# Optimization experiments

Hardware: AMD Instinct MI355X
Metric: run time of the kernel (lower is better)

## Reference

```python
import jax, jax.numpy as jnp
import numpy as np

B, N, DIM, T, H, DH = 4, 2048, 512, 16, 8, 64
EPS = 1e-5


def setup_inputs() -> dict:
    key = jax.random.key(0)
    ks = jax.random.split(key, 7)
    x = jax.random.normal(ks[0], (B, N, DIM), dtype=jnp.float32)
    # time-distance matrix, e.g. months between scans, in [0, 24)
    R = jax.random.uniform(ks[1], (B, T, T), dtype=jnp.float32) * 24.0
    gamma = jnp.ones((DIM,), dtype=jnp.float32)
    beta = jnp.zeros((DIM,), dtype=jnp.float32)
    W_qkv = jax.random.normal(ks[2], (DIM, 3 * H * DH), dtype=jnp.float32) * 0.02
    W_out = jax.random.normal(ks[3], (H * DH, DIM), dtype=jnp.float32) * 0.02
    a = jax.random.uniform(ks[4], (H,), dtype=jnp.float32)          # torch.rand(heads)
    c = 12.0 * jax.random.uniform(ks[5], (H,), dtype=jnp.float32)   # 12 * torch.rand(heads)
    return {"x": x, "R": R, "gamma": gamma, "beta": beta,
            "W_qkv": W_qkv, "W_out": W_out, "a": a, "c": c}


def reference(x, R, gamma, beta, W_qkv, W_out, a, c):
    b, n, dim = x.shape
    t = R.shape[-1]
    num_patches = n // t
    scale = DH ** -0.5

    # LayerNorm
    mu = jnp.mean(x, axis=-1, keepdims=True)
    var = jnp.mean(jnp.square(x - mu), axis=-1, keepdims=True)
    xn = (x - mu) * jax.lax.rsqrt(var + EPS) * gamma + beta

    # QKV projection -> [b, h, n, d]
    qkv = xn @ W_qkv  # [b, n, 3*h*d]
    q, k, v = jnp.split(qkv, 3, axis=-1)
    def to_heads(z):
        return z.reshape(b, n, H, DH).transpose(0, 2, 1, 3)
    q, k, v = to_heads(q), to_heads(k), to_heads(v)

    # attention scores with ReLU then learned sigmoid time-decay mask
    dots = jnp.einsum('bhnd,bhmd->bhnm', q, k) * scale
    dots = jax.nn.relu(dots)

    # flipped-sigmoid decay: 1 / (1 + exp(|a|*R - |c|)), per head  -> [b, h, t, t]
    decay = 1.0 / (1.0 + jnp.exp(jnp.abs(a)[None, :, None, None] * R[:, None, :, :]
                                 - jnp.abs(c)[None, :, None, None]))
    # expand timepoint mask to token resolution (repeat_interleave on both axes)
    decay = jnp.repeat(jnp.repeat(decay, num_patches, axis=2), num_patches, axis=3)

    attn = jax.nn.softmax(dots * decay, axis=-1)
    out = jnp.einsum('bhnm,bhmd->bhnd', attn, v)
    out = out.transpose(0, 2, 1, 3).reshape(b, n, H * DH)
    return out @ W_out  # dropout is identity at eval
```

## Files before the change

kernel.cpp:

```cpp
#include <hip/hip_runtime.h>
#include <math.h>

#define B_   4
#define N_   2048
#define DIM_ 512
#define T_   16
#define H_   8
#define DH_  64

typedef unsigned short ushort_t;
typedef __attribute__((ext_vector_type(8))) short bf16x8;
typedef __attribute__((ext_vector_type(16))) float f32x16;

__device__ inline ushort_t bf16_rn(float x) {
  unsigned u = __builtin_bit_cast(unsigned, x);
  u += 0x7FFFu + ((u >> 16) & 1u);
  return (ushort_t)(u >> 16);
}
__device__ inline float bf16f(ushort_t h) {
  return __builtin_bit_cast(float, (unsigned)h << 16);
}
__device__ inline unsigned pack2(ushort_t a, ushort_t b) {
  return (unsigned)a | ((unsigned)b << 16);
}
__device__ inline void split2(float x, ushort_t &h, ushort_t &l) {
  h = bf16_rn(x);
  l = bf16_rn(x - bf16f(h));
}

__global__ __launch_bounds__(256) void transpose_split_kernel(
    const float* __restrict__ src, ushort_t* __restrict__ dh,
    ushort_t* __restrict__ dl, int K, int Nn) {
  __shared__ float Ts[64][68];
  int tid = threadIdx.x;
  int n0 = blockIdx.x * 64;
  int k0 = blockIdx.y * 64;
#pragma unroll
  for (int it = 0; it < 4; ++it) {
    int idx = tid + it * 256;
    int r = idx >> 4, c4 = (idx & 15) * 4;
    *(float4*)&Ts[r][c4] = *(const float4*)&src[(size_t)(k0 + r) * Nn + n0 + c4];
  }
  __syncthreads();
#pragma unroll
  for (int it = 0; it < 2; ++it) {
    int idx = tid + it * 256;
    int n = idx >> 3, kc = (idx & 7) * 8;
    ushort_t hs[8], ls[8];
#pragma unroll
    for (int j = 0; j < 8; ++j) split2(Ts[kc + j][n], hs[j], ls[j]);
    uint4 uh, ul;
    uh.x = pack2(hs[0], hs[1]); uh.y = pack2(hs[2], hs[3]);
    uh.z = pack2(hs[4], hs[5]); uh.w = pack2(hs[6], hs[7]);
    ul.x = pack2(ls[0], ls[1]); ul.y = pack2(ls[2], ls[3]);
    ul.z = pack2(ls[4], ls[5]); ul.w = pack2(ls[6], ls[7]);
    size_t o = (size_t)(n0 + n) * K + k0 + kc;
    *(uint4*)&dh[o] = uh;
    *(uint4*)&dl[o] = ul;
  }
}

__global__ __launch_bounds__(256) void ln_xn_kernel(
    const float* __restrict__ x, const float* __restrict__ gamma,
    const float* __restrict__ beta, ushort_t* __restrict__ xnh,
    ushort_t* __restrict__ xnl) {
  int row  = blockIdx.x * 4 + (threadIdx.x >> 6);
  int lane = threadIdx.x & 63;
  const float4* xr = (const float4*)(x + (size_t)row * DIM_);
  float4 v0 = xr[lane * 2 + 0];
  float4 v1 = xr[lane * 2 + 1];
  float s  = v0.x + v0.y + v0.z + v0.w + v1.x + v1.y + v1.z + v1.w;
  float ss = v0.x*v0.x + v0.y*v0.y + v0.z*v0.z + v0.w*v0.w
           + v1.x*v1.x + v1.y*v1.y + v1.z*v1.z + v1.w*v1.w;
#pragma unroll
  for (int off = 32; off > 0; off >>= 1) {
    s  += __shfl_xor(s, off);
    ss += __shfl_xor(ss, off);
  }
  float mu  = s * (1.0f / DIM_);
  float var = ss * (1.0f / DIM_) - mu * mu;
  float rstd = rsqrtf(var + 1e-5f);
  float4 g0 = *(const float4*)&gamma[lane * 8];
  float4 g1 = *(const float4*)&gamma[lane * 8 + 4];
  float4 b0 = *(const float4*)&beta[lane * 8];
  float4 b1 = *(const float4*)&beta[lane * 8 + 4];
  float xv[8] = {v0.x, v0.y, v0.z, v0.w, v1.x, v1.y, v1.z, v1.w};
  float gv[8] = {g0.x, g0.y, g0.z, g0.w, g1.x, g1.y, g1.z, g1.w};
  float bv[8] = {b0.x, b0.y, b0.z, b0.w, b1.x, b1.y, b1.z, b1.w};
  ushort_t hs[8], ls[8];
#pragma unroll
  for (int j = 0; j < 8; ++j) {
    float xn = (xv[j] - mu) * rstd * gv[j] + bv[j];
    split2(xn, hs[j], ls[j]);
  }
  uint4 uh, ul;
  uh.x = pack2(hs[0], hs[1]); uh.y = pack2(hs[2], hs[3]);
  uh.z = pack2(hs[4], hs[5]); uh.w = pack2(hs[6], hs[7]);
  ul.x = pack2(ls[0], ls[1]); ul.y = pack2(ls[2], ls[3]);
  ul.z = pack2(ls[4], ls[5]); ul.w = pack2(ls[6], ls[7]);
  size_t o = (size_t)row * DIM_ + lane * 8;
  *(uint4*)&xnh[o] = uh;
  *(uint4*)&xnl[o] = ul;
}

__global__ __launch_bounds__(256) void qkv_gemm_mfma(
    const ushort_t* __restrict__ xnh, const ushort_t* __restrict__ xnl,
    const ushort_t* __restrict__ wth, const ushort_t* __restrict__ wtl,
    ushort_t* __restrict__ qh, ushort_t* __restrict__ ql,
    ushort_t* __restrict__ kho, ushort_t* __restrict__ klo,
    ushort_t* __restrict__ vt) {
  __shared__ ushort_t Ah[128 * 40], Al[128 * 40], Bh[128 * 40], Bl[128 * 40];
  int tid = threadIdx.x;
  int w = tid >> 6, lane = tid & 63, l31 = lane & 31, g = lane >> 5;
  int wm = w >> 1, wn = w & 1;
  int n0 = blockIdx.x * 128;
  int m0 = blockIdx.y * 128;

  f32x16 acc[2][2];
#pragma unroll
  for (int i = 0; i < 2; ++i)
#pragma unroll
    for (int j = 0; j < 2; ++j)
#pragma unroll
      for (int e = 0; e < 16; ++e) acc[i][j][e] = 0.0f;

  int fm[2], fc[2];
#pragma unroll
  for (int it = 0; it < 2; ++it) {
    int f = tid + it * 256;
    fm[it] = f >> 2;
    fc[it] = (f & 3) * 8;
  }

#pragma unroll 1
  for (int kt = 0; kt < 16; ++kt) {
    __syncthreads();
#pragma unroll
    for (int it = 0; it < 2; ++it) {
      size_t ao = (size_t)(m0 + fm[it]) * 512 + kt * 32 + fc[it];
      size_t bo = (size_t)(n0 + fm[it]) * 512 + kt * 32 + fc[it];
      uint4 tah = *(const uint4*)&xnh[ao];
      uint4 tal = *(const uint4*)&xnl[ao];
      uint4 tbh = *(const uint4*)&wth[bo];
      uint4 tbl = *(const uint4*)&wtl[bo];
      int o = fm[it] * 40 + fc[it];
      *(uint4*)&Ah[o] = tah;
      *(uint4*)&Al[o] = tal;
      *(uint4*)&Bh[o] = tbh;
      *(uint4*)&Bl[o] = tbl;
    }
    __syncthreads();
#pragma unroll
    for (int kc = 0; kc < 2; ++kc) {
      int off = kc * 16 + 8 * g;
      bf16x8 afh[2], afl[2], bfh[2], bfl[2];
#pragma unroll
      for (int rb = 0; rb < 2; ++rb) {
        int r = (wm * 64 + rb * 32 + l31) * 40 + off;
        afh[rb] = *(const bf16x8*)&Ah[r];
        afl[rb] = *(const bf16x8*)&Al[r];
      }
#pragma unroll
      for (int cb = 0; cb < 2; ++cb) {
        int r = (wn * 64 + cb * 32 + l31) * 40 + off;
        bfh[cb] = *(const bf16x8*)&Bh[r];
        bfl[cb] = *(const bf16x8*)&Bl[r];
      }
#pragma unroll
      for (int rb = 0; rb < 2; ++rb)
#pragma unroll
        for (int cb = 0; cb < 2; ++cb) {
          acc[rb][cb] = __builtin_amdgcn_mfma_f32_32x32x16_bf16(afh[rb], bfh[cb], acc[rb][cb], 0, 0, 0);
          acc[rb][cb] = __builtin_amdgcn_mfma_f32_32x32x16_bf16(afh[rb], bfl[cb], acc[rb][cb], 0, 0, 0);
          acc[rb][cb] = __builtin_amdgcn_mfma_f32_32x32x16_bf16(afl[rb], bfh[cb], acc[rb][cb], 0, 0, 0);
        }
    }
  }

  int part = n0 >> 9;
#pragma unroll
  for (int rb = 0; rb < 2; ++rb) {
    int m_base = m0 + wm * 64 + rb * 32;
#pragma unroll
    for (int cb = 0; cb < 2; ++cb) {
      int n_g = n0 + wn * 64 + cb * 32 + l31;
      int rem = n_g & 511, hh = rem >> 6, d = rem & 63;
      if (part == 2) {
#pragma unroll
        for (int grp = 0; grp < 4; ++grp) {
          int m_g = m_base + grp * 8 + 4 * g;
          int bb = m_g >> 11, tok = m_g & 2047;
          uint2 pk;
          pk.x = pack2(bf16_rn(acc[rb][cb][grp * 4 + 0]), bf16_rn(acc[rb][cb][grp * 4 + 1]));
          pk.y = pack2(bf16_rn(acc[rb][cb][grp * 4 + 2]), bf16_rn(acc[rb][cb][grp * 4 + 3]));
          *(uint2*)&vt[((size_t)(bb * 8 + hh) * 64 + d) * 2048 + tok] = pk;
        }
      } else {
        float sc = (part == 0) ? 0.125f : 1.0f;
        ushort_t* dsth = (part == 0) ? qh : kho;
        ushort_t* dstl = (part == 0) ? ql : klo;
#pragma unroll
        for (int reg = 0; reg < 16; ++reg) {
          int row = (reg & 3) + 8 * (reg >> 2) + 4 * g;
          int m_g = m_base + row;
          int bb = m_g >> 11, tok = m_g & 2047;
          ushort_t hi, lo;
          split2(acc[rb][cb][reg] * sc, hi, lo);
          size_t addr = ((size_t)(bb * 8 + hh) * 2048 + tok) * 64 + d;
          dsth[addr] = hi;
          dstl[addr] = lo;
        }
      }
    }
  }
}

__global__ __launch_bounds__(256) void attn_mfma(
    const ushort_t* __restrict__ qh, const ushort_t* __restrict__ ql,
    const ushort_t* __restrict__ kho, const ushort_t* __restrict__ klo,
    const ushort_t* __restrict__ vt, const float* __restrict__ R,
    const float* __restrict__ a, const float* __restrict__ c,
    ushort_t* __restrict__ aoh, ushort_t* __restrict__ aol) {
  __shared__ ushort_t KhS[64 * 72], KlS[64 * 72], VtS[64 * 72], PS[64 * 72];
  __shared__ float rsLDS[2][64];

  int tid = threadIdx.x;
  int w = tid >> 6, lane = tid & 63, l31 = lane & 31, g = lane >> 5;
  int qhalf = w >> 1, khalf = w & 1;
  int bh = blockIdx.x;
  int qt = blockIdx.y;
  int b = bh >> 3, h = bh & 7;
  float aab = fabsf(a[h]);
  float cab = fabsf(c[h]);

  size_t qoff = ((size_t)bh * 2048 + qt * 64 + qhalf * 32 + l31) * 64;
  bf16x8 qfh[4], qfl[4];
#pragma unroll
  for (int d0i = 0; d0i < 4; ++d0i) {
    qfh[d0i] = *(const bf16x8*)&qh[qoff + d0i * 16 + 8 * g];
    qfl[d0i] = *(const bf16x8*)&ql[qoff + d0i * 16 + 8 * g];
  }

  int frow[2], fcc[2];
#pragma unroll
  for (int it = 0; it < 2; ++it) {
    int f = tid + it * 256;
    frow[it] = f >> 3;
    fcc[it] = (f & 7) * 8;
  }
  const ushort_t* kbase = kho + (size_t)bh * 2048 * 64;
  const ushort_t* lbase = klo + (size_t)bh * 2048 * 64;
  const ushort_t* vbase = vt + (size_t)bh * 64 * 2048;

  f32x16 oacc;
#pragma unroll
  for (int i = 0; i < 16; ++i) oacc[i] = 0.0f;
  float rs_acc[16] = {};
  int ti = qt >> 1;

#pragma unroll 1
  for (int kt = 0; kt < 32; ++kt) {
    __syncthreads();
#pragma unroll
    for (int it = 0; it < 2; ++it) {
      uint4 tk = *(const uint4*)&kbase[(size_t)(kt * 64 + frow[it]) * 64 + fcc[it]];
      uint4 tl = *(const uint4*)&lbase[(size_t)(kt * 64 + frow[it]) * 64 + fcc[it]];
      uint4 tv = *(const uint4*)&vbase[(size_t)frow[it] * 2048 + kt * 64 + fcc[it]];
      int o = frow[it] * 72 + fcc[it];
      *(uint4*)&KhS[o] = tk;
      *(uint4*)&KlS[o] = tl;
      *(uint4*)&VtS[o] = tv;
    }
    __syncthreads();

    f32x16 sacc;
#pragma unroll
    for (int i = 0; i < 16; ++i) sacc[i] = 0.0f;
    int krow = (khalf * 32 + l31) * 72;
#pragma unroll
    for (int d0i = 0; d0i < 4; ++d0i) {
      int off = krow + d0i * 16 + 8 * g;
      bf16x8 kfh = *(const bf16x8*)&KhS[off];
      bf16x8 kfl = *(const bf16x8*)&KlS[off];
      sacc = __builtin_amdgcn_mfma_f32_32x32x16_bf16(qfh[d0i], kfh, sacc, 0, 0, 0);
      sacc = __builtin_amdgcn_mfma_f32_32x32x16_bf16(qfh[d0i], kfl, sacc, 0, 0, 0);
      sacc = __builtin_amdgcn_mfma_f32_32x32x16_bf16(qfl[d0i], kfh, sacc, 0, 0, 0);
    }

    float Rv = R[b * (T_ * T_) + ti * T_ + (kt >> 1)];
    float dec = 1.0f / (1.0f + __expf(aab * Rv - cab));
#pragma unroll
    for (int reg = 0; reg < 16; ++reg) {
      float pv = __expf(fmaxf(sacc[reg], 0.0f) * dec);
      rs_acc[reg] += pv;
      int row = (reg & 3) + 8 * (reg >> 2) + 4 * g;
      PS[(qhalf * 32 + row) * 72 + khalf * 32 + l31] = bf16_rn(pv);
    }
    __syncthreads();

#pragma unroll
    for (int k0i = 0; k0i < 4; ++k0i) {
      bf16x8 pf = *(const bf16x8*)&PS[(qhalf * 32 + l31) * 72 + k0i * 16 + 8 * g];
      bf16x8 vf = *(const bf16x8*)&VtS[(khalf * 32 + l31) * 72 + k0i * 16 + 8 * g];
      oacc = __builtin_amdgcn_mfma_f32_32x32x16_bf16(pf, vf, oacc, 0, 0, 0);
    }
  }

#pragma unroll
  for (int reg = 0; reg < 16; ++reg) {
    float vsum = rs_acc[reg];
    vsum += __shfl_xor(vsum, 1);
    vsum += __shfl_xor(vsum, 2);
    vsum += __shfl_xor(vsum, 4);
    vsum += __shfl_xor(vsum, 8);
    vsum += __shfl_xor(vsum, 16);
    rs_acc[reg] = vsum;
  }
  if (l31 == 0) {
#pragma unroll
    for (int reg = 0; reg < 16; ++reg) {
      int row = (reg & 3) + 8 * (reg >> 2) + 4 * g;
      rsLDS[khalf][qhalf * 32 + row] = rs_acc[reg];
    }
  }
  __syncthreads();

#pragma unroll
  for (int reg = 0; reg < 16; ++reg) {
    int row = (reg & 3) + 8 * (reg >> 2) + 4 * g;
    int qg = qhalf * 32 + row;
    float invs = 1.0f / (rsLDS[0][qg] + rsLDS[1][qg]);
    int tok = qt * 64 + qg;
    int d = khalf * 32 + l31;
    ushort_t hi, lo;
    split2(oacc[reg] * invs, hi, lo);
    size_t addr = ((size_t)b * 2048 + tok) * 512 + h * 64 + d;
    aoh[addr] = hi;
    aol[addr] = lo;
  }
}

__global__ __launch_bounds__(256) void out_gemm_mfma(
    const ushort_t* __restrict__ ah, const ushort_t* __restrict__ al,
    const ushort_t* __restrict__ wth, const ushort_t* __restrict__ wtl,
    float* __restrict__ out) {
  __shared__ ushort_t Ah[128 * 40], Al[128 * 40], Bh[128 * 40], Bl[128 * 40];
  int tid = threadIdx.x;
  int w = tid >> 6, lane = tid & 63, l31 = lane & 31, g = lane >> 5;
  int wm = w >> 1, wn = w & 1;
  int n0 = blockIdx.x * 128;
  int m0 = blockIdx.y * 128;

  f32x16 acc[2][2];
#pragma unroll
  for (int i = 0; i < 2; ++i)
#pragma unroll
    for (int j = 0; j < 2; ++j)
#pragma unroll
      for (int e = 0; e < 16; ++e) acc[i][j][e] = 0.0f;

  int fm[2], fc[2];
#pragma unroll
  for (int it = 0; it < 2; ++it) {
    int f = tid + it * 256;
    fm[it] = f >> 2;
    fc[it] = (f & 3) * 8;
  }

#pragma unroll 1
  for (int kt = 0; kt < 16; ++kt) {
    __syncthreads();
#pragma unroll
    for (int it = 0; it < 2; ++it) {
      size_t ao = (size_t)(m0 + fm[it]) * 512 + kt * 32 + fc[it];
      size_t bo = (size_t)(n0 + fm[it]) * 512 + kt * 32 + fc[it];
      uint4 tah = *(const uint4*)&ah[ao];
      uint4 tal = *(const uint4*)&al[ao];
      uint4 tbh = *(const uint4*)&wth[bo];
      uint4 tbl = *(const uint4*)&wtl[bo];
      int o = fm[it] * 40 + fc[it];
      *(uint4*)&Ah[o] = tah;
      *(uint4*)&Al[o] = tal;
      *(uint4*)&Bh[o] = tbh;
      *(uint4*)&Bl[o] = tbl;
    }
    __syncthreads();
#pragma unroll
    for (int kc = 0; kc < 2; ++kc) {
      int off = kc * 16 + 8 * g;
      bf16x8 afh[2], afl[2], bfh[2], bfl[2];
#pragma unroll
      for (int rb = 0; rb < 2; ++rb) {
        int r = (wm * 64 + rb * 32 + l31) * 40 + off;
        afh[rb] = *(const bf16x8*)&Ah[r];
        afl[rb] = *(const bf16x8*)&Al[r];
      }
#pragma unroll
      for (int cb = 0; cb < 2; ++cb) {
        int r = (wn * 64 + cb * 32 + l31) * 40 + off;
        bfh[cb] = *(const bf16x8*)&Bh[r];
        bfl[cb] = *(const bf16x8*)&Bl[r];
      }
#pragma unroll
      for (int rb = 0; rb < 2; ++rb)
#pragma unroll
        for (int cb = 0; cb < 2; ++cb) {
          acc[rb][cb] = __builtin_amdgcn_mfma_f32_32x32x16_bf16(afh[rb], bfh[cb], acc[rb][cb], 0, 0, 0);
          acc[rb][cb] = __builtin_amdgcn_mfma_f32_32x32x16_bf16(afh[rb], bfl[cb], acc[rb][cb], 0, 0, 0);
          acc[rb][cb] = __builtin_amdgcn_mfma_f32_32x32x16_bf16(afl[rb], bfh[cb], acc[rb][cb], 0, 0, 0);
        }
    }
  }

#pragma unroll
  for (int rb = 0; rb < 2; ++rb) {
    int m_base = m0 + wm * 64 + rb * 32;
#pragma unroll
    for (int cb = 0; cb < 2; ++cb) {
      int n_g = n0 + wn * 64 + cb * 32 + l31;
#pragma unroll
      for (int reg = 0; reg < 16; ++reg) {
        int row = (reg & 3) + 8 * (reg >> 2) + 4 * g;
        out[(size_t)(m_base + row) * 512 + n_g] = acc[rb][cb][reg];
      }
    }
  }
}

extern "C" void kernel_launch(void* const* d_in, const int* in_sizes, int n_in,
                              void* d_out, int out_size, void* d_ws, size_t ws_size,
                              hipStream_t stream) {
  (void)in_sizes; (void)n_in;
  const float* x     = (const float*)d_in[0];
  const float* R     = (const float*)d_in[1];
  const float* gamma = (const float*)d_in[2];
  const float* beta  = (const float*)d_in[3];
  const float* Wqkv  = (const float*)d_in[4];
  const float* Wout  = (const float*)d_in[5];
  const float* av    = (const float*)d_in[6];
  const float* cv    = (const float*)d_in[7];
  float* out = (float*)d_out;

  const size_t EL  = (size_t)B_ * N_ * DIM_;
  const size_t SZT = EL * sizeof(ushort_t);

  char* p = (char*)d_ws;
  ushort_t* wqh = (ushort_t*)p;                  p += (size_t)1536 * 512 * 2;
  ushort_t* wql = (ushort_t*)p;                  p += (size_t)1536 * 512 * 2;
  ushort_t* woh = (ushort_t*)p;                  p += (size_t)512 * 512 * 2;
  ushort_t* wol = (ushort_t*)p;                  p += (size_t)512 * 512 * 2;
  ushort_t* qhb = (ushort_t*)p;                  p += SZT;
  ushort_t* qlb = (ushort_t*)p;                  p += SZT;
  ushort_t* khb = (ushort_t*)p;                  p += SZT;
  ushort_t* klb = (ushort_t*)p;                  p += SZT;
  ushort_t* vtb = (ushort_t*)p;                  p += SZT;
  size_t base_need = (size_t)(p - (char*)d_ws);
  size_t needA = base_need + 2 * SZT;

  bool planA = (ws_size >= needA);
  ushort_t* xnh = planA ? (ushort_t*)p : (ushort_t*)d_out;
  ushort_t* xnl = xnh + EL;
  float* gemm_dst = planA ? out : (float*)qhb;

  transpose_split_kernel<<<dim3(24, 8), dim3(256), 0, stream>>>(Wqkv, wqh, wql, 512, 1536);
  transpose_split_kernel<<<dim3(8, 8), dim3(256), 0, stream>>>(Wout, woh, wol, 512, 512);
  ln_xn_kernel<<<dim3(2048), dim3(256), 0, stream>>>(x, gamma, beta, xnh, xnl);
  qkv_gemm_mfma<<<dim3(12, 64), dim3(256), 0, stream>>>(xnh, xnl, wqh, wql,
                                                        qhb, qlb, khb, klb, vtb);
  attn_mfma<<<dim3(32, 32), dim3(256), 0, stream>>>(qhb, qlb, khb, klb, vtb,
                                                    R, av, cv, xnh, xnl);
  out_gemm_mfma<<<dim3(4, 64), dim3(256), 0, stream>>>(xnh, xnl, woh, wol, gemm_dst);
  if (!planA) {
    hipMemcpyAsync(out, gemm_dst, (size_t)out_size * sizeof(float),
                   hipMemcpyDeviceToDevice, stream);
  }
}
```

Baseline: 263.7 us.

## Double-buffer GEMM and attention tiles with direct global-to-LDS loads and XOR swizzle

```diff
diff --git a/kernel.cpp b/kernel.cpp
--- a/kernel.cpp
+++ b/kernel.cpp
@@ -1,5 +1,6 @@
 #include <hip/hip_runtime.h>
 #include <math.h>
+#include <stdint.h>
 
 #define B_   4
 #define N_   2048
@@ -9,6 +10,7 @@
 #define DH_  64
 
 typedef unsigned short ushort_t;
+typedef unsigned int u32;
 typedef __attribute__((ext_vector_type(8))) short bf16x8;
 typedef __attribute__((ext_vector_type(16))) float f32x16;
 
@@ -26,6 +28,12 @@
 __device__ inline void split2(float x, ushort_t &h, ushort_t &l) {
   h = bf16_rn(x);
   l = bf16_rn(x - bf16f(h));
+}
+
+__device__ __forceinline__ void gld16(const ushort_t* g, ushort_t* s) {
+  __builtin_amdgcn_global_load_lds(
+      (const __attribute__((address_space(1))) u32*)(uintptr_t)g,
+      (__attribute__((address_space(3))) u32*)(uintptr_t)s, 16, 0, 0);
 }
 
 __global__ __launch_bounds__(256) void transpose_split_kernel(
@@ -109,12 +117,14 @@
     ushort_t* __restrict__ qh, ushort_t* __restrict__ ql,
     ushort_t* __restrict__ kho, ushort_t* __restrict__ klo,
     ushort_t* __restrict__ vt) {
-  __shared__ ushort_t Ah[128 * 40], Al[128 * 40], Bh[128 * 40], Bl[128 * 40];
+  __shared__ ushort_t AhS[2][128 * 32], AlS[2][128 * 32];
+  __shared__ ushort_t BhS[2][128 * 32], BlS[2][128 * 32];
   int tid = threadIdx.x;
   int w = tid >> 6, lane = tid & 63, l31 = lane & 31, g = lane >> 5;
   int wm = w >> 1, wn = w & 1;
   int n0 = blockIdx.x * 128;
   int m0 = blockIdx.y * 128;
+  int rl4 = lane >> 2, p4 = lane & 3;
 
   f32x16 acc[2][2];
 #pragma unroll
@@ -124,47 +134,55 @@
 #pragma unroll
       for (int e = 0; e < 16; ++e) acc[i][j][e] = 0.0f;
 
-  int fm[2], fc[2];
-#pragma unroll
-  for (int it = 0; it < 2; ++it) {
-    int f = tid + it * 256;
-    fm[it] = f >> 2;
-    fc[it] = (f & 3) * 8;
+  int offA[2][2], offB[2][2];
+#pragma unroll
+  for (int rb = 0; rb < 2; ++rb)
+#pragma unroll
+    for (int kc = 0; kc < 2; ++kc) {
+      int rA = wm * 64 + rb * 32 + l31;
+      int rB = wn * 64 + rb * 32 + l31;
+      offA[rb][kc] = rA * 32 + (((kc * 2 + g) ^ (rA & 3)) * 8);
+      offB[rb][kc] = rB * 32 + (((kc * 2 + g) ^ (rB & 3)) * 8);
+    }
+
+#pragma unroll
+  for (int i = 0; i < 2; ++i) {
+    int rbase = w * 32 + i * 16;
+    int row = rbase + rl4;
+    int c = p4 ^ (row & 3);
+    gld16(&xnh[(size_t)(m0 + row) * 512 + c * 8], &AhS[0][rbase * 32]);
+    gld16(&xnl[(size_t)(m0 + row) * 512 + c * 8], &AlS[0][rbase * 32]);
+    gld16(&wth[(size_t)(n0 + row) * 512 + c * 8], &BhS[0][rbase * 32]);
+    gld16(&wtl[(size_t)(n0 + row) * 512 + c * 8], &BlS[0][rbase * 32]);
   }
 
 #pragma unroll 1
   for (int kt = 0; kt < 16; ++kt) {
+    int cur = kt & 1, nxt = cur ^ 1;
     __syncthreads();
-#pragma unroll
-    for (int it = 0; it < 2; ++it) {
-      size_t ao = (size_t)(m0 + fm[it]) * 512 + kt * 32 + fc[it];
-      size_t bo = (size_t)(n0 + fm[it]) * 512 + kt * 32 + fc[it];
-      uint4 tah = *(const uint4*)&xnh[ao];
-      uint4 tal = *(const uint4*)&xnl[ao];
-      uint4 tbh = *(const uint4*)&wth[bo];
-      uint4 tbl = *(const uint4*)&wtl[bo];
-      int o = fm[it] * 40 + fc[it];
-      *(uint4*)&Ah[o] = tah;
-      *(uint4*)&Al[o] = tal;
-      *(uint4*)&Bh[o] = tbh;
-      *(uint4*)&Bl[o] = tbl;
-    }
-    __syncthreads();
+    int ktn = (kt + 1) & 15;
+#pragma unroll
+    for (int i = 0; i < 2; ++i) {
+      int rbase = w * 32 + i * 16;
+      int row = rbase + rl4;
+      int c = p4 ^ (row & 3);
+      gld16(&xnh[(size_t)(m0 + row) * 512 + ktn * 32 + c * 8], &AhS[nxt][rbase * 32]);
+      gld16(&xnl[(size_t)(m0 + row) * 512 + ktn * 32 + c * 8], &AlS[nxt][rbase * 32]);
+      gld16(&wth[(size_t)(n0 + row) * 512 + ktn * 32 + c * 8], &BhS[nxt][rbase * 32]);
+      gld16(&wtl[(size_t)(n0 + row) * 512 + ktn * 32 + c * 8], &BlS[nxt][rbase * 32]);
+    }
 #pragma unroll
     for (int kc = 0; kc < 2; ++kc) {
-      int off = kc * 16 + 8 * g;
       bf16x8 afh[2], afl[2], bfh[2], bfl[2];
 #pragma unroll
       for (int rb = 0; rb < 2; ++rb) {
-        int r = (wm * 64 + rb * 32 + l31) * 40 + off;
-        afh[rb] = *(const bf16x8*)&Ah[r];
-        afl[rb] = *(const bf16x8*)&Al[r];
+        afh[rb] = *(const bf16x8*)&AhS[cur][offA[rb][kc]];
+        afl[rb] = *(const bf16x8*)&AlS[cur][offA[rb][kc]];
       }
 #pragma unroll
       for (int cb = 0; cb < 2; ++cb) {
-        int r = (wn * 64 + cb * 32 + l31) * 40 + off;
-        bfh[cb] = *(const bf16x8*)&Bh[r];
-        bfl[cb] = *(const bf16x8*)&Bl[r];
+        bfh[cb] = *(const bf16x8*)&BhS[cur][offB[cb][kc]];
+        bfl[cb] = *(const bf16x8*)&BlS[cur][offB[cb][kc]];
       }
 #pragma unroll
       for (int rb = 0; rb < 2; ++rb)
@@ -221,7 +239,8 @@
     const ushort_t* __restrict__ vt, const float* __restrict__ R,
     const float* __restrict__ a, const float* __restrict__ c,
     ushort_t* __restrict__ aoh, ushort_t* __restrict__ aol) {
-  __shared__ ushort_t KhS[64 * 72], KlS[64 * 72], VtS[64 * 72], PS[64 * 72];
+  __shared__ ushort_t KhS[2][64 * 64], KlS[2][64 * 64], VtS[2][64 * 64];
+  __shared__ ushort_t PS[64 * 72];
   __shared__ float rsLDS[2][64];
 
   int tid = threadIdx.x;
@@ -232,6 +251,7 @@
   int b = bh >> 3, h = bh & 7;
   float aab = fabsf(a[h]);
   float cab = fabsf(c[h]);
+  int rl8 = lane >> 3, p8 = lane & 7;
 
   size_t qoff = ((size_t)bh * 2048 + qt * 64 + qhalf * 32 + l31) * 64;
   bf16x8 qfh[4], qfl[4];
@@ -241,17 +261,28 @@
     qfl[d0i] = *(const bf16x8*)&ql[qoff + d0i * 16 + 8 * g];
   }
 
-  int frow[2], fcc[2];
-#pragma unroll
-  for (int it = 0; it < 2; ++it) {
-    int f = tid + it * 256;
-    frow[it] = f >> 3;
-    fcc[it] = (f & 7) * 8;
-  }
   const ushort_t* kbase = kho + (size_t)bh * 2048 * 64;
   const ushort_t* lbase = klo + (size_t)bh * 2048 * 64;
   const ushort_t* vbase = vt + (size_t)bh * 64 * 2048;
 
+  int koff[4];
+  {
+    int r = khalf * 32 + l31;
+#pragma unroll
+    for (int d0i = 0; d0i < 4; ++d0i)
+      koff[d0i] = r * 64 + (((d0i * 2 + g) ^ (r & 7)) * 8);
+  }
+
+#pragma unroll
+  for (int i = 0; i < 2; ++i) {
+    int rbase = w * 16 + i * 8;
+    int row = rbase + rl8;
+    int cc = p8 ^ (row & 7);
+    gld16(&kbase[(size_t)row * 64 + cc * 8], &KhS[0][rbase * 64]);
+    gld16(&lbase[(size_t)row * 64 + cc * 8], &KlS[0][rbase * 64]);
+    gld16(&vbase[(size_t)row * 2048 + cc * 8], &VtS[0][rbase * 64]);
+  }
+
   f32x16 oacc;
 #pragma unroll
   for (int i = 0; i < 16; ++i) oacc[i] = 0.0f;
@@ -260,28 +291,26 @@
 
 #pragma unroll 1
   for (int kt = 0; kt < 32; ++kt) {
+    int cur = kt & 1, nxt = cur ^ 1;
     __syncthreads();
-#pragma unroll
-    for (int it = 0; it < 2; ++it) {
-      uint4 tk = *(const uint4*)&kbase[(size_t)(kt * 64 + frow[it]) * 64 + fcc[it]];
-      uint4 tl = *(const uint4*)&lbase[(size_t)(kt * 64 + frow[it]) * 64 + fcc[it]];
-      uint4 tv = *(const uint4*)&vbase[(size_t)frow[it] * 2048 + kt * 64 + fcc[it]];
-      int o = frow[it] * 72 + fcc[it];
-      *(uint4*)&KhS[o] = tk;
-      *(uint4*)&KlS[o] = tl;
-      *(uint4*)&VtS[o] = tv;
-    }
-    __syncthreads();
+    int ktn = (kt + 1) & 31;
+#pragma unroll
+    for (int i = 0; i < 2; ++i) {
+      int rbase = w * 16 + i * 8;
+      int row = rbase + rl8;
+      int cc = p8 ^ (row & 7);
+      gld16(&kbase[(size_t)(ktn * 64 + row) * 64 + cc * 8], &KhS[nxt][rbase * 64]);
+      gld16(&lbase[(size_t)(ktn * 64 + row) * 64 + cc * 8], &KlS[nxt][rbase * 64]);
+      gld16(&vbase[(size_t)row * 2048 + ktn * 64 + cc * 8], &VtS[nxt][rbase * 64]);
+    }
 
     f32x16 sacc;
 #pragma unroll
     for (int i = 0; i < 16; ++i) sacc[i] = 0.0f;
-    int krow = (khalf * 32 + l31) * 72;
 #pragma unroll
     for (int d0i = 0; d0i < 4; ++d0i) {
-      int off = krow + d0i * 16 + 8 * g;
-      bf16x8 kfh = *(const bf16x8*)&KhS[off];
-      bf16x8 kfl = *(const bf16x8*)&KlS[off];
+      bf16x8 kfh = *(const bf16x8*)&KhS[cur][koff[d0i]];
+      bf16x8 kfl = *(const bf16x8*)&KlS[cur][koff[d0i]];
       sacc = __builtin_amdgcn_mfma_f32_32x32x16_bf16(qfh[d0i], kfh, sacc, 0, 0, 0);
       sacc = __builtin_amdgcn_mfma_f32_32x32x16_bf16(qfh[d0i], kfl, sacc, 0, 0, 0);
       sacc = __builtin_amdgcn_mfma_f32_32x32x16_bf16(qfl[d0i], kfh, sacc, 0, 0, 0);
@@ -301,7 +330,7 @@
 #pragma unroll
     for (int k0i = 0; k0i < 4; ++k0i) {
       bf16x8 pf = *(const bf16x8*)&PS[(qhalf * 32 + l31) * 72 + k0i * 16 + 8 * g];
-      bf16x8 vf = *(const bf16x8*)&VtS[(khalf * 32 + l31) * 72 + k0i * 16 + 8 * g];
+      bf16x8 vf = *(const bf16x8*)&VtS[cur][koff[k0i]];
       oacc = __builtin_amdgcn_mfma_f32_32x32x16_bf16(pf, vf, oacc, 0, 0, 0);
     }
   }
@@ -344,12 +373,14 @@
     const ushort_t* __restrict__ ah, const ushort_t* __restrict__ al,
     const ushort_t* __restrict__ wth, const ushort_t* __restrict__ wtl,
     float* __restrict__ out) {
-  __shared__ ushort_t Ah[128 * 40], Al[128 * 40], Bh[128 * 40], Bl[128 * 40];
+  __shared__ ushort_t AhS[2][128 * 32], AlS[2][128 * 32];
+  __shared__ ushort_t BhS[2][128 * 32], BlS[2][128 * 32];
   int tid = threadIdx.x;
   int w = tid >> 6, lane = tid & 63, l31 = lane & 31, g = lane >> 5;
   int wm = w >> 1, wn = w & 1;
   int n0 = blockIdx.x * 128;
   int m0 = blockIdx.y * 128;
+  int rl4 = lane >> 2, p4 = lane & 3;
 
   f32x16 acc[2][2];
 #pragma unroll
@@ -359,47 +390,55 @@
 #pragma unroll
       for (int e = 0; e < 16; ++e) acc[i][j][e] = 0.0f;
 
-  int fm[2], fc[2];
-#pragma unroll
-  for (int it = 0; it < 2; ++it) {
-    int f = tid + it * 256;
-    fm[it] = f >> 2;
-    fc[it] = (f & 3) * 8;
+  int offA[2][2], offB[2][2];
+#pragma unroll
+  for (int rb = 0; rb < 2; ++rb)
+#pragma unroll
+    for (int kc = 0; kc < 2; ++kc) {
+      int rA = wm * 64 + rb * 32 + l31;
+      int rB = wn * 64 + rb * 32 + l31;
+      offA[rb][kc] = rA * 32 + (((kc * 2 + g) ^ (rA & 3)) * 8);
+      offB[rb][kc] = rB * 32 + (((kc * 2 + g) ^ (rB & 3)) * 8);
+    }
+
+#pragma unroll
+  for (int i = 0; i < 2; ++i) {
+    int rbase = w * 32 + i * 16;
+    int row = rbase + rl4;
+    int c = p4 ^ (row & 3);
+    gld16(&ah[(size_t)(m0 + row) * 512 + c * 8], &AhS[0][rbase * 32]);
+    gld16(&al[(size_t)(m0 + row) * 512 + c * 8], &AlS[0][rbase * 32]);
+    gld16(&wth[(size_t)(n0 + row) * 512 + c * 8], &BhS[0][rbase * 32]);
+    gld16(&wtl[(size_t)(n0 + row) * 512 + c * 8], &BlS[0][rbase * 32]);
   }
 
 #pragma unroll 1
   for (int kt = 0; kt < 16; ++kt) {
+    int cur = kt & 1, nxt = cur ^ 1;
     __syncthreads();
-#pragma unroll
-    for (int it = 0; it < 2; ++it) {
-      size_t ao = (size_t)(m0 + fm[it]) * 512 + kt * 32 + fc[it];
-      size_t bo = (size_t)(n0 + fm[it]) * 512 + kt * 32 + fc[it];
-      uint4 tah = *(const uint4*)&ah[ao];
-      uint4 tal = *(const uint4*)&al[ao];
-      uint4 tbh = *(const uint4*)&wth[bo];
-      uint4 tbl = *(const uint4*)&wtl[bo];
-      int o = fm[it] * 40 + fc[it];
-      *(uint4*)&Ah[o] = tah;
-      *(uint4*)&Al[o] = tal;
-      *(uint4*)&Bh[o] = tbh;
-      *(uint4*)&Bl[o] = tbl;
-    }
-    __syncthreads();
+    int ktn = (kt + 1) & 15;
+#pragma unroll
+    for (int i = 0; i < 2; ++i) {
+      int rbase = w * 32 + i * 16;
+      int row = rbase + rl4;
+      int c = p4 ^ (row & 3);
+      gld16(&ah[(size_t)(m0 + row) * 512 + ktn * 32 + c * 8], &AhS[nxt][rbase * 32]);
+      gld16(&al[(size_t)(m0 + row) * 512 + ktn * 32 + c * 8], &AlS[nxt][rbase * 32]);
+      gld16(&wth[(size_t)(n0 + row) * 512 + ktn * 32 + c * 8], &BhS[nxt][rbase * 32]);
+      gld16(&wtl[(size_t)(n0 + row) * 512 + ktn * 32 + c * 8], &BlS[nxt][rbase * 32]);
+    }
 #pragma unroll
     for (int kc = 0; kc < 2; ++kc) {
-      int off = kc * 16 + 8 * g;
       bf16x8 afh[2], afl[2], bfh[2], bfl[2];
 #pragma unroll
       for (int rb = 0; rb < 2; ++rb) {
-        int r = (wm * 64 + rb * 32 + l31) * 40 + off;
-        afh[rb] = *(const bf16x8*)&Ah[r];
-        afl[rb] = *(const bf16x8*)&Al[r];
+        afh[rb] = *(const bf16x8*)&AhS[cur][offA[rb][kc]];
+        afl[rb] = *(const bf16x8*)&AlS[cur][offA[rb][kc]];
       }
 #pragma unroll
       for (int cb = 0; cb < 2; ++cb) {
-        int r = (wn * 64 + cb * 32 + l31) * 40 + off;
-        bfh[cb] = *(const bf16x8*)&Bh[r];
-        bfl[cb] = *(const bf16x8*)&Bl[r];
+        bfh[cb] = *(const bf16x8*)&BhS[cur][offB[cb][kc]];
+        bfl[cb] = *(const bf16x8*)&BlS[cur][offB[cb][kc]];
       }
 #pragma unroll
       for (int rb = 0; rb < 2; ++rb)
```

Result: slower. 269.9 us (+2.4%).
